# Optimization experiments

Hardware: AMD Instinct MI355X
Metric: run time of the kernel (lower is better)

The kernel has to match this reference:

```python
import jax, jax.numpy as jnp
import numpy as np

WIN = 9           # local NCC window per axis
PAD = WIN // 2    # 'same' zero padding, matches F.conv3d(padding=4)
DN = ('NCDHW', 'OIDHW', 'NCDHW')


def box_sum(x):
    """9x9x9 local sum via separable 1D ones-filter convs (zero padding).
    Mathematically identical to conv3d with a 9^3 ones kernel."""
    for ax in range(3):
        kshape = [1, 1, 1, 1, 1]
        kshape[2 + ax] = WIN
        k = jnp.ones(kshape, x.dtype)
        pad = [(0, 0)] * 3
        pad[ax] = (PAD, PAD)
        x = jax.lax.conv_general_dilated(x, k, (1, 1, 1), pad, dimension_numbers=DN)
    return x


def nas_ncc(I, J):
    win_size = WIN ** 3
    I_sum = box_sum(I)
    J_sum = box_sum(J)
    I2_sum = box_sum(I * I)
    J2_sum = box_sum(J * J)
    IJ_sum = box_sum(I * J)
    u_I = I_sum / win_size
    u_J = J_sum / win_size
    cross = IJ_sum - u_J * I_sum - u_I * J_sum + u_I * u_J * win_size
    I_var = I2_sum - 2.0 * u_I * I_sum + u_I * u_I * win_size
    J_var = J2_sum - 2.0 * u_J * J_sum + u_J * u_J * win_size
    cc = cross * cross / (I_var * J_var + 1e-5)
    return -jnp.mean(cc)


def gradient_loss_l2(s):
    # finite differences along D, H, W of flow [B, 3, D, H, W]; l2 penalty
    dy = jnp.square(s[:, :, 1:, :, :] - s[:, :, :-1, :, :])
    dx = jnp.square(s[:, :, :, 1:, :] - s[:, :, :, :-1, :])
    dz = jnp.square(s[:, :, :, :, 1:] - s[:, :, :, :, :-1])
    return (jnp.mean(dx) + jnp.mean(dy) + jnp.mean(dz)) / 3.0


def setup_inputs() -> dict:
    key = jax.random.key(0)
    k1, k2, k3, k4 = jax.random.split(key, 4)
    shp = (1, 1, 160, 160, 160)
    return {
        'y': jax.random.normal(k1, shp, dtype=jnp.float32),
        'tgt': jax.random.normal(k2, shp, dtype=jnp.float32),
        'src': jax.random.normal(k3, shp, dtype=jnp.float32),
        'flow': jax.random.normal(k4, (1, 3, 160, 160, 160), dtype=jnp.float32),
    }


def reference(y, tgt, src, flow):
    hyper_1 = 10.0
    hyper_2 = 15.0
    ncc = nas_ncc(tgt, y)
    grad = gradient_loss_l2(flow)
    loss = hyper_1 * ncc + hyper_2 * grad
    return (loss, ncc, grad)
```

## Files before the change

kernel.cpp:

```cpp
#include <hip/hip_runtime.h>

#define DIM 160
#define PLANE 25600
#define NVOX 4096000
constexpr float INV_WS = 1.0f / 729.0f;

#define TW 32
#define TH 16
#define DC 16
#define HW 40
#define HH 24
#define PSTR 41
#define WSTR 33

#define NCC_WAVES 4000
#define GRAD_WAVES 1200

__global__ __launch_bounds__(512)
void ncc_fused_kernel(const float* __restrict__ I, const float* __restrict__ J,
                      double* __restrict__ part) {
    __shared__ float prod[5][HH * PSTR];
    __shared__ float wsum[5][HH * WSTR];
    __shared__ float hcol[5][TH * WSTR];

    const int tid = threadIdx.x;
    const int w0 = blockIdx.x * TW;
    const int h0 = blockIdx.y * TH;
    const int d0 = blockIdx.z * DC;
    const int wi = tid & 31;
    const int hi = tid >> 5;

    const int r0 = tid / HW, c0 = tid - r0 * HW;
    const int p1 = tid + 512;
    const int r1 = p1 / HW, c1 = p1 - r1 * HW;
    const int gr0 = h0 - 4 + r0, gc0 = w0 - 4 + c0;
    const int gr1 = h0 - 4 + r1, gc1 = w0 - 4 + c1;
    const bool v0 = (gr0 >= 0 && gr0 < DIM && gc0 >= 0 && gc0 < DIM);
    const bool v1 = (p1 < HH * HW) && (gr1 >= 0 && gr1 < DIM && gc1 >= 0 && gc1 < DIM);
    const int off0 = gr0 * DIM + gc0;
    const int off1 = gr1 * DIM + gc1;

    const int wt_f    = tid / 48;
    const int wt_rem  = tid - wt_f * 48;
    const int wt_r    = wt_rem >> 1;
    const int wt_base = (wt_rem & 1) * 16;

    const int ht_f = tid >> 5;
    const int ht_w = tid & 31;

    float S[5][9];
    #pragma unroll
    for (int f = 0; f < 5; ++f)
        #pragma unroll
        for (int s = 0; s < 9; ++s) S[f][s] = 0.f;
    float R[5] = {0.f, 0.f, 0.f, 0.f, 0.f};
    float local = 0.f;

    for (int k0 = 0; k0 < DC + 8; k0 += 9) {
        #pragma unroll
        for (int j = 0; j < 9; ++j) {
            const int k = k0 + j;
            if (k < DC + 8) {
                const int ds = d0 - 4 + k;
                if (ds >= 0 && ds < DIM) {
                    const int sb = ds * PLANE;
                    {
                        float a = 0.f, b = 0.f;
                        if (v0) { a = I[sb + off0]; b = J[sb + off0]; }
                        const int o = r0 * PSTR + c0;
                        prod[0][o] = a; prod[1][o] = b;
                        prod[2][o] = a * a; prod[3][o] = b * b; prod[4][o] = a * b;
                        if (p1 < HH * HW) {
                            float a1 = 0.f, b1 = 0.f;
                            if (v1) { a1 = I[sb + off1]; b1 = J[sb + off1]; }
                            const int o1 = r1 * PSTR + c1;
                            prod[0][o1] = a1; prod[1][o1] = b1;
                            prod[2][o1] = a1 * a1; prod[3][o1] = b1 * b1; prod[4][o1] = a1 * b1;
                        }
                    }
                    __syncthreads();
                    if (tid < 240) {
                        float c[24];
                        #pragma unroll
                        for (int q = 0; q < 24; ++q)
                            c[q] = prod[wt_f][wt_r * PSTR + wt_base + q];
                        float s = c[0]+c[1]+c[2]+c[3]+c[4]+c[5]+c[6]+c[7]+c[8];
                        wsum[wt_f][wt_r * WSTR + wt_base] = s;
                        #pragma unroll
                        for (int q = 1; q < 16; ++q) {
                            s += c[q + 8] - c[q - 1];
                            wsum[wt_f][wt_r * WSTR + wt_base + q] = s;
                        }
                    }
                    __syncthreads();
                    if (tid < 160) {
                        float c[24];
                        #pragma unroll
                        for (int q = 0; q < 24; ++q)
                            c[q] = wsum[ht_f][q * WSTR + ht_w];
                        float s = c[0]+c[1]+c[2]+c[3]+c[4]+c[5]+c[6]+c[7]+c[8];
                        hcol[ht_f][ht_w] = s;
                        #pragma unroll
                        for (int q = 1; q < 16; ++q) {
                            s += c[q + 8] - c[q - 1];
                            hcol[ht_f][q * WSTR + ht_w] = s;
                        }
                    }
                    __syncthreads();
                    #pragma unroll
                    for (int f = 0; f < 5; ++f) {
                        float P = hcol[f][hi * WSTR + wi];
                        R[f] += P - S[f][j];
                        S[f][j] = P;
                    }
                } else {
                    #pragma unroll
                    for (int f = 0; f < 5; ++f) { R[f] -= S[f][j]; S[f][j] = 0.f; }
                }
                if (k >= 8) {
                    float cross = R[4] - R[0] * R[1] * INV_WS;
                    float Iv    = R[2] - R[0] * R[0] * INV_WS;
                    float Jv    = R[3] - R[1] * R[1] * INV_WS;
                    local += cross * cross / (Iv * Jv + 1e-5f);
                }
            }
        }
    }

    for (int off = 32; off; off >>= 1) local += __shfl_down(local, off);
    if ((tid & 63) == 0) {
        int wave = ((blockIdx.z * gridDim.y + blockIdx.y) * gridDim.x + blockIdx.x) * 8
                 + (tid >> 6);
        part[wave] = (double)local;
    }
}

__global__ void grad_kernel(const float* __restrict__ s, double* __restrict__ part) {
    const int Q = NVOX / 4;
    const float4* s4 = (const float4*)s;
    const int w4 = blockIdx.x * 8 + (threadIdx.x & 7);
    const int h  = blockIdx.y * 32 + (threadIdx.x >> 3);
    const int c  = blockIdx.z >> 2;
    const int d0 = (blockIdx.z & 3) * 40;
    const int qbase = c * Q + h * (DIM / 4) + w4;

    float local = 0.f;
    float4 v = s4[qbase + d0 * (PLANE / 4)];
    for (int step = 0; step < 40; ++step) {
        const int d = d0 + step;
        const int qi = qbase + d * (PLANE / 4);
        float t;
        t = v.y - v.x; local += t * t;
        t = v.z - v.y; local += t * t;
        t = v.w - v.z; local += t * t;
        if (w4 < DIM / 4 - 1) {
            float nx = s[(qi + 1) * 4];
            t = nx - v.w; local += t * t;
        }
        if (h < DIM - 1) {
            float4 vh = s4[qi + DIM / 4];
            t = vh.x - v.x; local += t * t;
            t = vh.y - v.y; local += t * t;
            t = vh.z - v.z; local += t * t;
            t = vh.w - v.w; local += t * t;
        }
        if (d < DIM - 1) {
            float4 vn = s4[qi + PLANE / 4];
            t = vn.x - v.x; local += t * t;
            t = vn.y - v.y; local += t * t;
            t = vn.z - v.z; local += t * t;
            t = vn.w - v.w; local += t * t;
            v = vn;
        }
    }

    for (int off = 32; off; off >>= 1) local += __shfl_down(local, off);
    if ((threadIdx.x & 63) == 0) {
        int linear = (blockIdx.z * gridDim.y + blockIdx.y) * gridDim.x + blockIdx.x;
        part[NCC_WAVES + linear * 4 + (threadIdx.x >> 6)] = (double)local;
    }
}

__global__ void final_kernel(const double* __restrict__ part, float* __restrict__ out) {
    __shared__ double s_n[4], s_g[4];
    double n = 0.0, g = 0.0;
    for (int i = threadIdx.x; i < NCC_WAVES; i += 256) n += part[i];
    for (int i = threadIdx.x; i < GRAD_WAVES; i += 256) g += part[NCC_WAVES + i];
    for (int off = 32; off; off >>= 1) {
        n += __shfl_down(n, off);
        g += __shfl_down(g, off);
    }
    if ((threadIdx.x & 63) == 0) {
        s_n[threadIdx.x >> 6] = n;
        s_g[threadIdx.x >> 6] = g;
    }
    __syncthreads();
    if (threadIdx.x == 0) {
        double ncc_sum  = s_n[0] + s_n[1] + s_n[2] + s_n[3];
        double grad_sum = s_g[0] + s_g[1] + s_g[2] + s_g[3];
        double ncc  = -(ncc_sum / 4096000.0);
        double grad = grad_sum / 36633600.0;
        double loss = 10.0 * ncc + 15.0 * grad;
        out[0] = (float)loss;
        out[1] = (float)ncc;
        out[2] = (float)grad;
    }
}

extern "C" void kernel_launch(void* const* d_in, const int* in_sizes, int n_in,
                              void* d_out, int out_size, void* d_ws, size_t ws_size,
                              hipStream_t stream) {
    const float* y    = (const float*)d_in[0];
    const float* tgt  = (const float*)d_in[1];
    const float* flow = (const float*)d_in[3];
    float* out = (float*)d_out;
    double* part = (double*)d_ws;

    dim3 g1(DIM / TW, DIM / TH, DIM / DC);
    ncc_fused_kernel<<<g1, 512, 0, stream>>>(tgt, y, part);
    dim3 g2(5, 5, 12);
    grad_kernel<<<g2, 256, 0, stream>>>(flow, part);
    final_kernel<<<1, 256, 0, stream>>>(part, out);
}
```

Baseline: 205.4 us.

## Fuse NCC and gradient kernels into one launch and alias hcol onto prod smem

Merges the NCC box-sum kernel and the flow gradient kernel into a single launch, splitting the grid so the first 500 blocks do NCC and the next 500 do a grid-stride gradient reduction. The intent is to let the bandwidth-bound gradient work overlap with the NCC blocks and to drop one kernel launch. The hcol buffer now shares shared memory with prod, which cuts LDS per block to raise occupancy; an extra barrier per slice is added to keep that reuse safe. The gradient path now recomputes indices with divisions for every element and reads each D neighbour separately instead of reusing it, which adds integer work and memory traffic.

```diff
diff --git a/kernel.cpp b/kernel.cpp
--- a/kernel.cpp
+++ b/kernel.cpp
@@ -13,171 +13,173 @@
 #define PSTR 41
 #define WSTR 33
 
+#define NCC_BLOCKS 500
+#define GRAD_BLOCKS 500
 #define NCC_WAVES 4000
-#define GRAD_WAVES 1200
+#define GRAD_WAVES 4000
 
 __global__ __launch_bounds__(512)
-void ncc_fused_kernel(const float* __restrict__ I, const float* __restrict__ J,
-                      double* __restrict__ part) {
-    __shared__ float prod[5][HH * PSTR];
+void fused_kernel(const float* __restrict__ I, const float* __restrict__ J,
+                  const float* __restrict__ flow, double* __restrict__ part) {
+    __shared__ float prodA[5][HH * PSTR];
     __shared__ float wsum[5][HH * WSTR];
-    __shared__ float hcol[5][TH * WSTR];
+    float (*hcol)[TH * WSTR] = (float (*)[TH * WSTR]) & prodA[0][0];
 
     const int tid = threadIdx.x;
-    const int w0 = blockIdx.x * TW;
-    const int h0 = blockIdx.y * TH;
-    const int d0 = blockIdx.z * DC;
-    const int wi = tid & 31;
-    const int hi = tid >> 5;
-
-    const int r0 = tid / HW, c0 = tid - r0 * HW;
-    const int p1 = tid + 512;
-    const int r1 = p1 / HW, c1 = p1 - r1 * HW;
-    const int gr0 = h0 - 4 + r0, gc0 = w0 - 4 + c0;
-    const int gr1 = h0 - 4 + r1, gc1 = w0 - 4 + c1;
-    const bool v0 = (gr0 >= 0 && gr0 < DIM && gc0 >= 0 && gc0 < DIM);
-    const bool v1 = (p1 < HH * HW) && (gr1 >= 0 && gr1 < DIM && gc1 >= 0 && gc1 < DIM);
-    const int off0 = gr0 * DIM + gc0;
-    const int off1 = gr1 * DIM + gc1;
-
-    const int wt_f    = tid / 48;
-    const int wt_rem  = tid - wt_f * 48;
-    const int wt_r    = wt_rem >> 1;
-    const int wt_base = (wt_rem & 1) * 16;
-
-    const int ht_f = tid >> 5;
-    const int ht_w = tid & 31;
-
-    float S[5][9];
-    #pragma unroll
-    for (int f = 0; f < 5; ++f)
+
+    if (blockIdx.x < NCC_BLOCKS) {
+        const int b  = blockIdx.x;
+        const int bx = b % 5;
+        const int by = (b / 5) % 10;
+        const int bz = b / 50;
+        const int w0 = bx * TW;
+        const int h0 = by * TH;
+        const int d0 = bz * DC;
+        const int wi = tid & 31;
+        const int hi = tid >> 5;
+
+        const int r0 = tid / HW, c0 = tid - r0 * HW;
+        const int p1 = tid + 512;
+        const int r1 = p1 / HW, c1 = p1 - r1 * HW;
+        const int gr0 = h0 - 4 + r0, gc0 = w0 - 4 + c0;
+        const int gr1 = h0 - 4 + r1, gc1 = w0 - 4 + c1;
+        const bool v0 = (gr0 >= 0 && gr0 < DIM && gc0 >= 0 && gc0 < DIM);
+        const bool v1 = (p1 < HH * HW) && (gr1 >= 0 && gr1 < DIM && gc1 >= 0 && gc1 < DIM);
+        const int off0 = gr0 * DIM + gc0;
+        const int off1 = gr1 * DIM + gc1;
+
+        const int wt_f    = tid / 48;
+        const int wt_rem  = tid - wt_f * 48;
+        const int wt_r    = wt_rem >> 1;
+        const int wt_base = (wt_rem & 1) * 16;
+
+        const int ht_f = tid >> 5;
+        const int ht_w = tid & 31;
+
+        float S[5][9];
         #pragma unroll
-        for (int s = 0; s < 9; ++s) S[f][s] = 0.f;
-    float R[5] = {0.f, 0.f, 0.f, 0.f, 0.f};
-    float local = 0.f;
-
-    for (int k0 = 0; k0 < DC + 8; k0 += 9) {
-        #pragma unroll
-        for (int j = 0; j < 9; ++j) {
-            const int k = k0 + j;
-            if (k < DC + 8) {
-                const int ds = d0 - 4 + k;
-                if (ds >= 0 && ds < DIM) {
-                    const int sb = ds * PLANE;
-                    {
-                        float a = 0.f, b = 0.f;
-                        if (v0) { a = I[sb + off0]; b = J[sb + off0]; }
-                        const int o = r0 * PSTR + c0;
-                        prod[0][o] = a; prod[1][o] = b;
-                        prod[2][o] = a * a; prod[3][o] = b * b; prod[4][o] = a * b;
-                        if (p1 < HH * HW) {
-                            float a1 = 0.f, b1 = 0.f;
-                            if (v1) { a1 = I[sb + off1]; b1 = J[sb + off1]; }
-                            const int o1 = r1 * PSTR + c1;
-                            prod[0][o1] = a1; prod[1][o1] = b1;
-                            prod[2][o1] = a1 * a1; prod[3][o1] = b1 * b1; prod[4][o1] = a1 * b1;
-                        }
+        for (int f = 0; f < 5; ++f)
+            #pragma unroll
+            for (int s = 0; s < 9; ++s) S[f][s] = 0.f;
+        float R[5] = {0.f, 0.f, 0.f, 0.f, 0.f};
+        float local = 0.f;
+
+        for (int k0 = 0; k0 < DC + 8; k0 += 9) {
+            #pragma unroll
+            for (int j = 0; j < 9; ++j) {
+                const int k = k0 + j;
+                if (k < DC + 8) {
+                    const int ds = d0 - 4 + k;
+                    if (ds >= 0 && ds < DIM) {
+                        const int sb = ds * PLANE;
+                        __syncthreads();
+                        {
+                            float a = 0.f, bb = 0.f;
+                            if (v0) { a = I[sb + off0]; bb = J[sb + off0]; }
+                            const int o = r0 * PSTR + c0;
+                            prodA[0][o] = a; prodA[1][o] = bb;
+                            prodA[2][o] = a * a; prodA[3][o] = bb * bb; prodA[4][o] = a * bb;
+                            if (p1 < HH * HW) {
+                                float a1 = 0.f, b1 = 0.f;
+                                if (v1) { a1 = I[sb + off1]; b1 = J[sb + off1]; }
+                                const int o1 = r1 * PSTR + c1;
+                                prodA[0][o1] = a1; prodA[1][o1] = b1;
+                                prodA[2][o1] = a1 * a1; prodA[3][o1] = b1 * b1; prodA[4][o1] = a1 * b1;
+                            }
+                        }
+                        __syncthreads();
+                        if (tid < 240) {
+                            float c[24];
+                            #pragma unroll
+                            for (int q = 0; q < 24; ++q)
+                                c[q] = prodA[wt_f][wt_r * PSTR + wt_base + q];
+                            float s = c[0]+c[1]+c[2]+c[3]+c[4]+c[5]+c[6]+c[7]+c[8];
+                            wsum[wt_f][wt_r * WSTR + wt_base] = s;
+                            #pragma unroll
+                            for (int q = 1; q < 16; ++q) {
+                                s += c[q + 8] - c[q - 1];
+                                wsum[wt_f][wt_r * WSTR + wt_base + q] = s;
+                            }
+                        }
+                        __syncthreads();
+                        if (tid < 160) {
+                            float c[24];
+                            #pragma unroll
+                            for (int q = 0; q < 24; ++q)
+                                c[q] = wsum[ht_f][q * WSTR + ht_w];
+                            float s = c[0]+c[1]+c[2]+c[3]+c[4]+c[5]+c[6]+c[7]+c[8];
+                            hcol[ht_f][ht_w] = s;
+                            #pragma unroll
+                            for (int q = 1; q < 16; ++q) {
+                                s += c[q + 8] - c[q - 1];
+                                hcol[ht_f][q * WSTR + ht_w] = s;
+                            }
+                        }
+                        __syncthreads();
+                        #pragma unroll
+                        for (int f = 0; f < 5; ++f) {
+                            float P = hcol[f][hi * WSTR + wi];
+                            R[f] += P - S[f][j];
+                            S[f][j] = P;
+                        }
+                    } else {
+                        #pragma unroll
+                        for (int f = 0; f < 5; ++f) { R[f] -= S[f][j]; S[f][j] = 0.f; }
                     }
-                    __syncthreads();
-                    if (tid < 240) {
-                        float c[24];
-                        #pragma unroll
-                        for (int q = 0; q < 24; ++q)
-                            c[q] = prod[wt_f][wt_r * PSTR + wt_base + q];
-                        float s = c[0]+c[1]+c[2]+c[3]+c[4]+c[5]+c[6]+c[7]+c[8];
-                        wsum[wt_f][wt_r * WSTR + wt_base] = s;
-                        #pragma unroll
-                        for (int q = 1; q < 16; ++q) {
-                            s += c[q + 8] - c[q - 1];
-                            wsum[wt_f][wt_r * WSTR + wt_base + q] = s;
-                        }
+                    if (k >= 8) {
+                        float cross = R[4] - R[0] * R[1] * INV_WS;
+                        float Iv    = R[2] - R[0] * R[0] * INV_WS;
+                        float Jv    = R[3] - R[1] * R[1] * INV_WS;
+                        local += cross * cross / (Iv * Jv + 1e-5f);
                     }
-                    __syncthreads();
-                    if (tid < 160) {
-                        float c[24];
-                        #pragma unroll
-                        for (int q = 0; q < 24; ++q)
-                            c[q] = wsum[ht_f][q * WSTR + ht_w];
-                        float s = c[0]+c[1]+c[2]+c[3]+c[4]+c[5]+c[6]+c[7]+c[8];
-                        hcol[ht_f][ht_w] = s;
-                        #pragma unroll
-                        for (int q = 1; q < 16; ++q) {
-                            s += c[q + 8] - c[q - 1];
-                            hcol[ht_f][q * WSTR + ht_w] = s;
-                        }
-                    }
-                    __syncthreads();
-                    #pragma unroll
-                    for (int f = 0; f < 5; ++f) {
-                        float P = hcol[f][hi * WSTR + wi];
-                        R[f] += P - S[f][j];
-                        S[f][j] = P;
-                    }
-                } else {
-                    #pragma unroll
-                    for (int f = 0; f < 5; ++f) { R[f] -= S[f][j]; S[f][j] = 0.f; }
                 }
-                if (k >= 8) {
-                    float cross = R[4] - R[0] * R[1] * INV_WS;
-                    float Iv    = R[2] - R[0] * R[0] * INV_WS;
-                    float Jv    = R[3] - R[1] * R[1] * INV_WS;
-                    local += cross * cross / (Iv * Jv + 1e-5f);
-                }
-            }
-        }
-    }
-
-    for (int off = 32; off; off >>= 1) local += __shfl_down(local, off);
-    if ((tid & 63) == 0) {
-        int wave = ((blockIdx.z * gridDim.y + blockIdx.y) * gridDim.x + blockIdx.x) * 8
-                 + (tid >> 6);
-        part[wave] = (double)local;
-    }
-}
-
-__global__ void grad_kernel(const float* __restrict__ s, double* __restrict__ part) {
-    const int Q = NVOX / 4;
-    const float4* s4 = (const float4*)s;
-    const int w4 = blockIdx.x * 8 + (threadIdx.x & 7);
-    const int h  = blockIdx.y * 32 + (threadIdx.x >> 3);
-    const int c  = blockIdx.z >> 2;
-    const int d0 = (blockIdx.z & 3) * 40;
-    const int qbase = c * Q + h * (DIM / 4) + w4;
-
-    float local = 0.f;
-    float4 v = s4[qbase + d0 * (PLANE / 4)];
-    for (int step = 0; step < 40; ++step) {
-        const int d = d0 + step;
-        const int qi = qbase + d * (PLANE / 4);
-        float t;
-        t = v.y - v.x; local += t * t;
-        t = v.z - v.y; local += t * t;
-        t = v.w - v.z; local += t * t;
-        if (w4 < DIM / 4 - 1) {
-            float nx = s[(qi + 1) * 4];
-            t = nx - v.w; local += t * t;
-        }
-        if (h < DIM - 1) {
-            float4 vh = s4[qi + DIM / 4];
-            t = vh.x - v.x; local += t * t;
-            t = vh.y - v.y; local += t * t;
-            t = vh.z - v.z; local += t * t;
-            t = vh.w - v.w; local += t * t;
-        }
-        if (d < DIM - 1) {
-            float4 vn = s4[qi + PLANE / 4];
-            t = vn.x - v.x; local += t * t;
-            t = vn.y - v.y; local += t * t;
-            t = vn.z - v.z; local += t * t;
-            t = vn.w - v.w; local += t * t;
-            v = vn;
-        }
-    }
-
-    for (int off = 32; off; off >>= 1) local += __shfl_down(local, off);
-    if ((threadIdx.x & 63) == 0) {
-        int linear = (blockIdx.z * gridDim.y + blockIdx.y) * gridDim.x + blockIdx.x;
-        part[NCC_WAVES + linear * 4 + (threadIdx.x >> 6)] = (double)local;
+            }
+        }
+
+        for (int off = 32; off; off >>= 1) local += __shfl_down(local, off);
+        if ((tid & 63) == 0) {
+            part[b * 8 + (tid >> 6)] = (double)local;
+        }
+    } else {
+        const int Q = NVOX / 4;
+        const float4* s4 = (const float4*)flow;
+        const int gb = blockIdx.x - NCC_BLOCKS;
+        float local = 0.f;
+        for (int i = gb * 512 + tid; i < 3 * Q; i += GRAD_BLOCKS * 512) {
+            int c    = i / Q;
+            int rem  = i - c * Q;
+            int w4   = rem % (DIM / 4);
+            int rest = rem / (DIM / 4);
+            int h = rest % DIM;
+            int d = rest / DIM;
+            float4 v = s4[i];
+            float t;
+            t = v.y - v.x; local += t * t;
+            t = v.z - v.y; local += t * t;
+            t = v.w - v.z; local += t * t;
+            if (w4 < DIM / 4 - 1) {
+                float nx = flow[i * 4 + 4];
+                t = nx - v.w; local += t * t;
+            }
+            if (h < DIM - 1) {
+                float4 vh = s4[i + DIM / 4];
+                t = vh.x - v.x; local += t * t;
+                t = vh.y - v.y; local += t * t;
+                t = vh.z - v.z; local += t * t;
+                t = vh.w - v.w; local += t * t;
+            }
+            if (d < DIM - 1) {
+                float4 vd = s4[i + PLANE / 4];
+                t = vd.x - v.x; local += t * t;
+                t = vd.y - v.y; local += t * t;
+                t = vd.z - v.z; local += t * t;
+                t = vd.w - v.w; local += t * t;
+            }
+        }
+        for (int off = 32; off; off >>= 1) local += __shfl_down(local, off);
+        if ((tid & 63) == 0) {
+            part[NCC_WAVES + gb * 8 + (tid >> 6)] = (double)local;
+        }
     }
 }
 
@@ -216,9 +218,6 @@
     float* out = (float*)d_out;
     double* part = (double*)d_ws;
 
-    dim3 g1(DIM / TW, DIM / TH, DIM / DC);
-    ncc_fused_kernel<<<g1, 512, 0, stream>>>(tgt, y, part);
-    dim3 g2(5, 5, 12);
-    grad_kernel<<<g2, 256, 0, stream>>>(flow, part);
+    fused_kernel<<<NCC_BLOCKS + GRAD_BLOCKS, 512, 0, stream>>>(tgt, y, flow, part);
     final_kernel<<<1, 256, 0, stream>>>(part, out);
 }
```

Result: faster. 179.2 us (-12.7%).
